# Kernel tuning notes

Hardware: AMD Instinct MI355X
Metric: run time of the kernel (lower is better)

## Reference

```python
import jax, jax.numpy as jnp
import numpy as np

T, B, N, DEG, F_IN, H, C = 48, 32, 96, 8, 16, 128, 500
E = B * N * DEG          # edges per timestep (already batch-offset within [0, B*N))
M = T * B * N            # total nodes across all timesteps
EPS = 1e-5               # BatchNorm eps


def setup_inputs() -> dict:
    key = jax.random.key(0)
    ks = jax.random.split(key, 24)
    rn = lambda k, s: jax.random.normal(k, s, dtype=jnp.float32) * 0.05
    return {
        "x": jax.random.normal(ks[0], (T, B * N, F_IN), dtype=jnp.float32),
        "edge_index": jax.random.randint(ks[1], (T, 2, E), 0, B * N, dtype=jnp.int32),
        "gcn_w0": rn(ks[2], (F_IN, H)),
        "gcn_w12": rn(ks[3], (2, H, H)),
        "gcn_b": rn(ks[4], (3, H)),
        "bn_gamma": jnp.ones((3, H), dtype=jnp.float32),
        "bn_beta": jnp.zeros((3, H), dtype=jnp.float32),
        "bn_mean": rn(ks[5], (3, H)),
        "bn_var": jax.random.uniform(ks[6], (3, H), minval=0.5, maxval=1.5, dtype=jnp.float32),
        "lstm_wih0": rn(ks[7], (2, 4 * H, H)),
        "lstm_whh0": rn(ks[8], (2, 4 * H, H)),
        "lstm_bih0": rn(ks[9], (2, 4 * H)),
        "lstm_bhh0": rn(ks[10], (2, 4 * H)),
        "lstm_wih1": rn(ks[11], (2, 4 * H, 2 * H)),
        "lstm_whh1": rn(ks[12], (2, 4 * H, H)),
        "lstm_bih1": rn(ks[13], (2, 4 * H)),
        "lstm_bhh1": rn(ks[14], (2, 4 * H)),
        "attn_w1": rn(ks[15], (2 * H, H)),
        "attn_b1": rn(ks[16], (H,)),
        "attn_w2": rn(ks[17], (H, 1)),
        "attn_b2": rn(ks[18], (1,)),
        "fc1_w": rn(ks[19], (2 * H, H)),
        "fc1_b": rn(ks[20], (H,)),
        "fc2_w": rn(ks[21], (H, C)),
        "fc2_b": rn(ks[22], (C,)),
    }


def _lstm_dir(x, wih, whh, bih, bhh):
    # x: [T, B, I]; PyTorch gate order i, f, g, o
    pre = jnp.einsum('tbi,gi->tbg', x, wih) + bih  # input projection hoisted out of scan
    h0 = jnp.zeros((x.shape[1], whh.shape[1]), x.dtype)

    def step(carry, p):
        h, c = carry
        g = p + h @ whh.T + bhh
        i, f, gg, o = jnp.split(g, 4, axis=-1)
        c = jax.nn.sigmoid(f) * c + jax.nn.sigmoid(i) * jnp.tanh(gg)
        h = jax.nn.sigmoid(o) * jnp.tanh(c)
        return (h, c), h

    _, hs = jax.lax.scan(step, (h0, h0), pre)
    return hs  # [T, B, Hh]


def _bilstm(x, wih, whh, bih, bhh):
    fwd = _lstm_dir(x, wih[0], whh[0], bih[0], bhh[0])
    bwd = _lstm_dir(x[::-1], wih[1], whh[1], bih[1], bhh[1])[::-1]
    return jnp.concatenate([fwd, bwd], axis=-1)  # [T, B, 2H]


def reference(x, edge_index, gcn_w0, gcn_w12, gcn_b,
              bn_gamma, bn_beta, bn_mean, bn_var,
              lstm_wih0, lstm_whh0, lstm_bih0, lstm_bhh0,
              lstm_wih1, lstm_whh1, lstm_bih1, lstm_bhh1,
              attn_w1, attn_b1, attn_w2, attn_b2,
              fc1_w, fc1_b, fc2_w, fc2_b):
    # Fold timesteps into one big node set by offsetting indices by t*B*N
    off = (jnp.arange(T, dtype=jnp.int32) * (B * N))[:, None]
    src = (edge_index[:, 0] + off).reshape(-1)
    dst = (edge_index[:, 1] + off).reshape(-1)

    # GCN symmetric norm with self-loops: deg counts incoming edges + self-loop
    deg = jax.ops.segment_sum(jnp.ones_like(src, dtype=x.dtype), dst, num_segments=M) + 1.0
    dinv = jax.lax.rsqrt(deg)
    enorm = (dinv[src] * dinv[dst])[:, None]   # per-edge norm
    self_norm = (1.0 / deg)[:, None]           # self-loop norm

    h = x.reshape(M, F_IN)
    for l in range(3):
        W = gcn_w0 if l == 0 else gcn_w12[l - 1]
        hw = h @ W  # GCNConv applies linear first
        z = jax.ops.segment_sum(hw[src] * enorm, dst, num_segments=M) + hw * self_norm + gcn_b[l]
        # BatchNorm1d eval-mode (running stats), then ReLU, residual if shapes match
        z = (z - bn_mean[l]) * (bn_gamma[l] * jax.lax.rsqrt(bn_var[l] + EPS)) + bn_beta[l]
        z = jax.nn.relu(z)
        h = z + h if l > 0 else z  # dropout is identity in eval

    # global_mean_pool per graph (fixed N nodes per graph)
    emb = h.reshape(T, B, N, H).mean(axis=2)  # [T, B, H]

    out1 = _bilstm(emb, lstm_wih0, lstm_whh0, lstm_bih0, lstm_bhh0)
    out2 = _bilstm(out1, lstm_wih1, lstm_whh1, lstm_bih1, lstm_bhh1)
    lstm_out = out2.transpose(1, 0, 2)  # [B, T, 2H]

    a = jnp.tanh(lstm_out @ attn_w1 + attn_b1) @ attn_w2 + attn_b2  # [B, T, 1]
    w = jax.nn.softmax(a, axis=1)
    ws = jnp.sum(lstm_out * w, axis=1)  # [B, 2H]

    y = jax.nn.relu(ws @ fc1_w + fc1_b) @ fc2_w + fc2_b
    return jax.nn.log_softmax(y, axis=1)
```

## Files before the change

### kernel.cpp

```cpp
#include <hip/hip_runtime.h>

#define T_ 48
#define B_ 32
#define N_ 96
#define E_ 24576
#define BN_ (B_*N_)
#define M_ (T_*BN_)
#define FIN_ 16
#define H_ 128
#define C_ 500
#define TE_ (T_*E_)
#define EPS_ 1e-5f

typedef _Float16 f16x8 __attribute__((ext_vector_type(8)));
typedef float    f32x4 __attribute__((ext_vector_type(4)));
typedef _Float16 half2v __attribute__((ext_vector_type(2)));

__device__ __forceinline__ ushort f2h(float f) {
    _Float16 h = (_Float16)f;
    union { _Float16 h; ushort u; } v;
    v.h = h;
    return v.u;
}
__device__ __forceinline__ float h2f(ushort u) {
    union { ushort u; _Float16 h; } v;
    v.u = u;
    return (float)v.h;
}
__device__ __forceinline__ half2v pkfma(unsigned int v, unsigned int w, half2v acc) {
#if __has_builtin(__builtin_elementwise_fma)
    return __builtin_elementwise_fma(__builtin_bit_cast(half2v, v),
                                     __builtin_bit_cast(half2v, w), acc);
#else
    half2v hv = __builtin_bit_cast(half2v, v);
    half2v wv = __builtin_bit_cast(half2v, w);
    acc[0] += hv[0]*wv[0];
    acc[1] += hv[1]*wv[1];
    return acc;
#endif
}
__device__ __forceinline__ float dot2pk(unsigned int hbits, unsigned int wbits, float acc) {
#if __has_builtin(__builtin_amdgcn_fdot2)
    return __builtin_amdgcn_fdot2(__builtin_bit_cast(half2v, hbits),
                                  __builtin_bit_cast(half2v, wbits), acc, false);
#else
    half2v hv = __builtin_bit_cast(half2v, hbits);
    half2v wv = __builtin_bit_cast(half2v, wbits);
    acc = fmaf((float)hv[0], (float)wv[0], acc);
    acc = fmaf((float)hv[1], (float)wv[1], acc);
    return acc;
#endif
}
__device__ __forceinline__ float sigm(float x) {
    return 1.f / (1.f + __expf(-x));
}
__device__ __forceinline__ float ftanh(float x) {
    x = fminf(15.f, fmaxf(-15.f, x));
    float e = __expf(2.f * x);
    return (e - 1.f) / (e + 1.f);
}

__global__ __launch_bounds__(1024) void csr_build_k(
    const int* __restrict__ ei, int* __restrict__ csr_off,
    unsigned int* __restrict__ csr_pk, float* __restrict__ dinv)
{
    int t = blockIdx.x;
    int tid = threadIdx.x;
    __shared__ int cnt[BN_];
    __shared__ int cur[BN_];
    __shared__ int scanbuf[1024];
    __shared__ unsigned int pk[E_];

    #pragma unroll
    for (int i = 0; i < 3; i++) cnt[tid + i*1024] = 0;
    __syncthreads();

    const int* srcp = ei + ((long)t*2+0)*E_;
    const int* dstp = ei + ((long)t*2+1)*E_;
    #pragma unroll
    for (int i = 0; i < E_/1024; i++)
        atomicAdd(&cnt[dstp[tid + i*1024]], 1);
    __syncthreads();

    int n0 = tid*3;
    int a = cnt[n0], b = cnt[n0+1], c = cnt[n0+2];
    int tot = a + b + c;
    scanbuf[tid] = tot;
    __syncthreads();
    for (int d = 1; d < 1024; d <<= 1) {
        int add = (tid >= d) ? scanbuf[tid-d] : 0;
        __syncthreads();
        scanbuf[tid] += add;
        __syncthreads();
    }
    int excl = scanbuf[tid] - tot;
    cur[n0] = excl; cur[n0+1] = excl + a; cur[n0+2] = excl + a + b;
    int gbase = t*BN_, ebase = t*E_;
    csr_off[gbase+n0]   = ebase + excl;
    csr_off[gbase+n0+1] = ebase + excl + a;
    csr_off[gbase+n0+2] = ebase + excl + a + b;
    dinv[gbase+n0]   = rsqrtf((float)a + 1.f);
    dinv[gbase+n0+1] = rsqrtf((float)b + 1.f);
    dinv[gbase+n0+2] = rsqrtf((float)c + 1.f);
    if (t == T_-1 && tid == 0) csr_off[M_] = TE_;
    __syncthreads();

    #pragma unroll
    for (int i = 0; i < E_/1024; i++) {
        int e = tid + i*1024;
        int s = srcp[e], d = dstp[e];
        int pos = atomicAdd(&cur[d], 1);
        float w = rsqrtf((float)cnt[s] + 1.f) * rsqrtf((float)cnt[d] + 1.f);
        pk[pos] = (unsigned int)s | ((unsigned int)f2h(w) << 16);
    }
    __syncthreads();

    uint4* dpk = (uint4*)(csr_pk + ebase);
    const uint4* spk = (const uint4*)pk;
    #pragma unroll
    for (int i = 0; i < E_/4096; i++)
        dpk[tid + i*1024] = spk[tid + i*1024];
}

#define WPREP_TOTAL (384+1024+4096+16384+16384+65536+65536+131072+262144)
__global__ void wprep_k(
    const float* __restrict__ gcn_b, const float* __restrict__ gam,
    const float* __restrict__ bet, const float* __restrict__ mu,
    const float* __restrict__ var,
    float* __restrict__ bn_sc, float* __restrict__ bn_sh,
    const float* __restrict__ bih0, const float* __restrict__ bhh0,
    float* __restrict__ bias0,
    const float* __restrict__ bih1, const float* __restrict__ bhh1,
    float* __restrict__ bias1,
    const float* __restrict__ gcn_w0, const float* __restrict__ gcn_w12,
    ushort* __restrict__ w0t, ushort* __restrict__ w1t, ushort* __restrict__ w2t,
    const float* __restrict__ whh0, const float* __restrict__ whh1,
    unsigned int* __restrict__ wpk0, unsigned int* __restrict__ wpk1,
    const float* __restrict__ wih0, const float* __restrict__ wih1,
    ushort* __restrict__ wih0b, ushort* __restrict__ wih1b)
{
    int i = blockIdx.x * blockDim.x + threadIdx.x;
    if (i >= WPREP_TOTAL) return;
    if (i < 384) {
        float sc = gam[i] * rsqrtf(var[i] + EPS_);
        bn_sc[i] = sc;
        bn_sh[i] = gcn_b[i]*sc + bet[i] - mu[i]*sc;
        return;
    }
    i -= 384;
    if (i < 1024) {
        bias0[i] = bih0[i] + bhh0[i];
        bias1[i] = bih1[i] + bhh1[i];
        return;
    }
    i -= 1024;
    if (i < 4096) {
        int e = i & 7, lane = (i >> 3) & 63, ct = i >> 9;
        int k = (lane >> 4)*8 + e;
        int c = ct*16 + (lane & 15);
        w0t[i] = (k < 16) ? f2h(gcn_w0[k*128 + c]) : (ushort)0;
        return;
    }
    i -= 4096;
    if (i < 16384) {
        int e = i & 7, lane = (i >> 3) & 63, kk = (i >> 9) & 3, ct = i >> 11;
        int k = kk*32 + (lane >> 4)*8 + e;
        int c = ct*16 + (lane & 15);
        w1t[i] = f2h(gcn_w12[k*128 + c]);
        return;
    }
    i -= 16384;
    if (i < 16384) {
        int e = i & 7, lane = (i >> 3) & 63, kk = (i >> 9) & 3, ct = i >> 11;
        int k = kk*32 + (lane >> 4)*8 + e;
        int c = ct*16 + (lane & 15);
        w2t[i] = f2h(gcn_w12[16384 + k*128 + c]);
        return;
    }
    i -= 16384;
    if (i < 65536) {
        int dir = i >> 15, r = i & 32767;
        int ab = r >> 14, r2 = r & 16383;
        int q = r2 >> 8, tidw = r2 & 255;
        int hh = tidw >> 1, gp = tidw & 1;
        int g = (2*gp + ab)*128 + hh;
        const float* wr = whh0 + ((long)(dir*512 + g))*128 + 2*q;
        wpk0[i] = (unsigned int)f2h(wr[0]) | ((unsigned int)f2h(wr[1]) << 16);
        return;
    }
    i -= 65536;
    if (i < 65536) {
        int dir = i >> 15, r = i & 32767;
        int ab = r >> 14, r2 = r & 16383;
        int q = r2 >> 8, tidw = r2 & 255;
        int hh = tidw >> 1, gp = tidw & 1;
        int g = (2*gp + ab)*128 + hh;
        const float* wr = whh1 + ((long)(dir*512 + g))*128 + 2*q;
        wpk1[i] = (unsigned int)f2h(wr[0]) | ((unsigned int)f2h(wr[1]) << 16);
        return;
    }
    i -= 65536;
    if (i < 131072) {
        int dir = i >> 16, r = i & 0xFFFF;
        int nt = r >> 11, kk = (r >> 9) & 3, lane = (r >> 3) & 63, e = r & 7;
        int n = nt*16 + (lane & 15);
        int k = kk*32 + (lane >> 4)*8 + e;
        wih0b[i] = f2h(wih0[((long)dir*512 + n)*128 + k]);
        return;
    }
    i -= 131072;
    {
        int dir = i >> 17, r = i & 0x1FFFF;
        int nt = r >> 12, kk = (r >> 9) & 7, lane = (r >> 3) & 63, e = r & 7;
        int n = nt*16 + (lane & 15);
        int k = kk*32 + (lane >> 4)*8 + e;
        wih1b[i] = f2h(wih1[((long)dir*512 + n)*256 + k]);
    }
}

__global__ __launch_bounds__(256) void gcn_layer_k(
    const ushort* __restrict__ h, const ushort* __restrict__ Wt,
    ushort* __restrict__ Cout,
    const int* __restrict__ csr_off, const unsigned int* __restrict__ csr_pk,
    const float* __restrict__ dinv,
    const float* __restrict__ bnsc, const float* __restrict__ bnsh)
{
    __shared__ ushort agg[64][136];
    int nb = gridDim.x;
    int chunk = nb >> 3;
    int bswz = (blockIdx.x & 7) * chunk + (blockIdx.x >> 3);
    int base = bswz * 64;
    int tbase = (base / BN_) * BN_;
    int wv = threadIdx.x >> 6;
    int lane = threadIdx.x & 63;
    int l2 = lane * 2;

    for (int pass = 0; pass < 8; pass++) {
        int nodeA = __builtin_amdgcn_readfirstlane(base + pass*8 + wv*2);
        int e00 = __builtin_amdgcn_readfirstlane(csr_off[nodeA]);
        int e01 = __builtin_amdgcn_readfirstlane(csr_off[nodeA+1]);
        int e11 = __builtin_amdgcn_readfirstlane(csr_off[nodeA+2]);
        int dA = e01 - e00, dB = e11 - e01;
        unsigned int mypkA = (lane < dA) ? csr_pk[e00 + lane] : 0u;
        unsigned int mypkB = (lane < dB) ? csr_pk[e01 + lane] : 0u;
        float dvA = dinv[nodeA], dvB = dinv[nodeA+1];
        unsigned int selfA = *(const unsigned int*)(h + (size_t)nodeA*128 + l2);
        unsigned int selfB = *(const unsigned int*)(h + (size_t)(nodeA+1)*128 + l2);

        ushort swA = f2h(dvA * dvA), swB = f2h(dvB * dvB);
        half2v spA = __builtin_bit_cast(half2v, (unsigned int)(swA * 0x10001u));
        half2v spB = __builtin_bit_cast(half2v, (unsigned int)(swB * 0x10001u));
        half2v a0 = __builtin_bit_cast(half2v, selfA);
        a0[0] *= spA[0]; a0[1] *= spA[1];
        half2v b0 = __builtin_bit_cast(half2v, selfB);
        b0[0] *= spB[0]; b0[1] *= spB[1];
        half2v a1 = {(_Float16)0.f, (_Float16)0.f}, a2 = a1, a3 = a1;
        half2v b1 = a1, b2 = a1, b3 = a1;

        int cA = (dA < 64) ? dA : 64;
        int cB = (dB < 64) ? dB : 64;
        int cA4 = cA & ~3, cB4 = cB & ~3;
        int cm = (cA4 > cB4) ? cA4 : cB4;
        for (int j = 0; j < cm; j += 4) {
            unsigned int pA0, pA1, pA2, pA3, vA0, vA1, vA2, vA3;
            unsigned int pB0, pB1, pB2, pB3, vB0, vB1, vB2, vB3;
            bool qA = (j < cA4), qB = (j < cB4);
            if (qA) {
                pA0 = (unsigned int)__builtin_amdgcn_readlane((int)mypkA, j+0);
                pA1 = (unsigned int)__builtin_amdgcn_readlane((int)mypkA, j+1);
                pA2 = (unsigned int)__builtin_amdgcn_readlane((int)mypkA, j+2);
                pA3 = (unsigned int)__builtin_amdgcn_readlane((int)mypkA, j+3);
                vA0 = *(const unsigned int*)(h + (size_t)(tbase + (int)(pA0 & 0xffffu))*128 + l2);
                vA1 = *(const unsigned int*)(h + (size_t)(tbase + (int)(pA1 & 0xffffu))*128 + l2);
                vA2 = *(const unsigned int*)(h + (size_t)(tbase + (int)(pA2 & 0xffffu))*128 + l2);
                vA3 = *(const unsigned int*)(h + (size_t)(tbase + (int)(pA3 & 0xffffu))*128 + l2);
            }
            if (qB) {
                pB0 = (unsigned int)__builtin_amdgcn_readlane((int)mypkB, j+0);
                pB1 = (unsigned int)__builtin_amdgcn_readlane((int)mypkB, j+1);
                pB2 = (unsigned int)__builtin_amdgcn_readlane((int)mypkB, j+2);
                pB3 = (unsigned int)__builtin_amdgcn_readlane((int)mypkB, j+3);
                vB0 = *(const unsigned int*)(h + (size_t)(tbase + (int)(pB0 & 0xffffu))*128 + l2);
                vB1 = *(const unsigned int*)(h + (size_t)(tbase + (int)(pB1 & 0xffffu))*128 + l2);
                vB2 = *(const unsigned int*)(h + (size_t)(tbase + (int)(pB2 & 0xffffu))*128 + l2);
                vB3 = *(const unsigned int*)(h + (size_t)(tbase + (int)(pB3 & 0xffffu))*128 + l2);
            }
            if (qA) {
                a0 = pkfma(vA0, (pA0 >> 16) * 0x10001u, a0);
                a1 = pkfma(vA1, (pA1 >> 16) * 0x10001u, a1);
                a2 = pkfma(vA2, (pA2 >> 16) * 0x10001u, a2);
                a3 = pkfma(vA3, (pA3 >> 16) * 0x10001u, a3);
            }
            if (qB) {
                b0 = pkfma(vB0, (pB0 >> 16) * 0x10001u, b0);
                b1 = pkfma(vB1, (pB1 >> 16) * 0x10001u, b1);
                b2 = pkfma(vB2, (pB2 >> 16) * 0x10001u, b2);
                b3 = pkfma(vB3, (pB3 >> 16) * 0x10001u, b3);
            }
        }
        for (int j = cA4; j < cA; j++) {
            unsigned int pk0 = (unsigned int)__builtin_amdgcn_readlane((int)mypkA, j);
            unsigned int v = *(const unsigned int*)(h + (size_t)(tbase + (int)(pk0 & 0xffffu))*128 + l2);
            a0 = pkfma(v, (pk0 >> 16) * 0x10001u, a0);
        }
        for (int j = cB4; j < cB; j++) {
            unsigned int pk0 = (unsigned int)__builtin_amdgcn_readlane((int)mypkB, j);
            unsigned int v = *(const unsigned int*)(h + (size_t)(tbase + (int)(pk0 & 0xffffu))*128 + l2);
            b0 = pkfma(v, (pk0 >> 16) * 0x10001u, b0);
        }
        for (int jj = e00 + 64; jj < e01; jj++) {
            unsigned int pk0 = __builtin_amdgcn_readfirstlane(csr_pk[jj]);
            unsigned int v = *(const unsigned int*)(h + (size_t)(tbase + (int)(pk0 & 0xffffu))*128 + l2);
            a0 = pkfma(v, (pk0 >> 16) * 0x10001u, a0);
        }
        for (int jj = e01 + 64; jj < e11; jj++) {
            unsigned int pk0 = __builtin_amdgcn_readfirstlane(csr_pk[jj]);
            unsigned int v = *(const unsigned int*)(h + (size_t)(tbase + (int)(pk0 & 0xffffu))*128 + l2);
            b0 = pkfma(v, (pk0 >> 16) * 0x10001u, b0);
        }
        float ra0 = ((float)a0[0] + (float)a1[0]) + ((float)a2[0] + (float)a3[0]);
        float ra1 = ((float)a0[1] + (float)a1[1]) + ((float)a2[1] + (float)a3[1]);
        float rb0 = ((float)b0[0] + (float)b1[0]) + ((float)b2[0] + (float)b3[0]);
        float rb1 = ((float)b0[1] + (float)b1[1]) + ((float)b2[1] + (float)b3[1]);
        int nlA = nodeA - base;
        *(unsigned int*)&agg[nlA][l2] =
            (unsigned int)f2h(ra0) | ((unsigned int)f2h(ra1) << 16);
        *(unsigned int*)&agg[nlA+1][l2] =
            (unsigned int)f2h(rb0) | ((unsigned int)f2h(rb1) << 16);
    }
    __syncthreads();

    int l16 = lane & 15, lh = lane >> 4;
    f32x4 acc[8];
    #pragma unroll
    for (int i = 0; i < 8; i++) acc[i] = (f32x4){0.f, 0.f, 0.f, 0.f};
    #pragma unroll
    for (int kk = 0; kk < 4; kk++) {
        f16x8 af = *reinterpret_cast<const f16x8*>(&agg[wv*16 + l16][kk*32 + lh*8]);
        #pragma unroll
        for (int ct = 0; ct < 8; ct++) {
            f16x8 bfr = *reinterpret_cast<const f16x8*>(
                &Wt[(((long)ct*4 + kk)*64 + lane)*8]);
            acc[ct] = __builtin_amdgcn_mfma_f32_16x16x32_f16(af, bfr, acc[ct], 0, 0, 0);
        }
    }
    __syncthreads();

    #pragma unroll
    for (int ct = 0; ct < 8; ct++) {
        int col = ct*16 + l16;
        float sc = bnsc[col], sh = bnsh[col];
        #pragma unroll
        for (int r = 0; r < 4; r++) {
            int rl = wv*16 + lh*4 + r;
            float v = acc[ct][r] * sc + sh;
            agg[rl][col] = f2h(fmaxf(v, 0.f));
        }
    }
    __syncthreads();
    long rowblock = (long)base;
    #pragma unroll
    for (int it = 0; it < 4; it++) {
        int s = it*256 + threadIdx.x;
        int rl = s >> 4, c8 = (s & 15) * 8;
        uint4 v = *(const uint4*)&agg[rl][c8];
        uint4 rv = *(const uint4*)&h[(rowblock + rl)*128 + c8];
        half2v* vv = (half2v*)&v;
        const half2v* rr = (const half2v*)&rv;
        vv[0] += rr[0]; vv[1] += rr[1]; vv[2] += rr[2]; vv[3] += rr[3];
        *(uint4*)&Cout[(rowblock + rl)*128 + c8] = v;
    }
}

__global__ __launch_bounds__(256) void gcn0_k(
    const float* __restrict__ x, const ushort* __restrict__ Wt,
    ushort* __restrict__ Cout,
    const int* __restrict__ csr_off, const unsigned int* __restrict__ csr_pk,
    const float* __restrict__ dinv,
    const float* __restrict__ bnsc, const float* __restrict__ bnsh)
{
    __shared__ ushort agg[64][32];
    __shared__ ushort cl[64][136];
    int tid = threadIdx.x;
    int nl = tid >> 2;
    int fq = tid & 3;
    int f0 = fq*4;
    int node = blockIdx.x*64 + nl;
    int tbase = (node / BN_) * BN_;
    float dv = dinv[node];
    float4 sv = *(const float4*)(x + (long)node*16 + f0);
    float s = dv*dv;
    float a0 = sv.x*s, a1 = sv.y*s, a2 = sv.z*s, a3 = sv.w*s;
    int e0 = csr_off[node], e1 = csr_off[node+1];
    int j = e0;
    for (; j + 4 <= e1; j += 4) {
        unsigned int p0 = csr_pk[j], p1 = csr_pk[j+1], p2 = csr_pk[j+2], p3 = csr_pk[j+3];
        int s0 = tbase + (int)(p0 & 0xffffu), s1 = tbase + (int)(p1 & 0xffffu);
        int s2 = tbase + (int)(p2 & 0xffffu), s3 = tbase + (int)(p3 & 0xffffu);
        float w0 = h2f((ushort)(p0 >> 16)), w1 = h2f((ushort)(p1 >> 16));
        float w2 = h2f((ushort)(p2 >> 16)), w3 = h2f((ushort)(p3 >> 16));
        float4 v0 = *(const float4*)(x + (long)s0*16 + f0);
        float4 v1 = *(const float4*)(x + (long)s1*16 + f0);
        float4 v2 = *(const float4*)(x + (long)s2*16 + f0);
        float4 v3 = *(const float4*)(x + (long)s3*16 + f0);
        a0 += v0.x*w0 + v1.x*w1 + v2.x*w2 + v3.x*w3;
        a1 += v0.y*w0 + v1.y*w1 + v2.y*w2 + v3.y*w3;
        a2 += v0.z*w0 + v1.z*w1 + v2.z*w2 + v3.z*w3;
        a3 += v0.w*w0 + v1.w*w1 + v2.w*w2 + v3.w*w3;
    }
    for (; j < e1; j++) {
        unsigned int pk0 = csr_pk[j];
        int sc = tbase + (int)(pk0 & 0xffffu);
        float en = h2f((ushort)(pk0 >> 16));
        float4 v = *(const float4*)(x + (long)sc*16 + f0);
        a0 += v.x*en; a1 += v.y*en; a2 += v.z*en; a3 += v.w*en;
    }
    agg[nl][f0+0] = f2h(a0);
    agg[nl][f0+1] = f2h(a1);
    agg[nl][f0+2] = f2h(a2);
    agg[nl][f0+3] = f2h(a3);
    agg[nl][16+f0+0] = 0;
    agg[nl][16+f0+1] = 0;
    agg[nl][16+f0+2] = 0;
    agg[nl][16+f0+3] = 0;
    __syncthreads();

    int w = tid >> 6, lane = tid & 63;
    int l16 = lane & 15, lh = lane >> 4;
    f16x8 af = *reinterpret_cast<const f16x8*>(&agg[w*16 + l16][lh*8]);
    f32x4 acc[8];
    #pragma unroll
    for (int i = 0; i < 8; i++) acc[i] = (f32x4){0.f, 0.f, 0.f, 0.f};
    #pragma unroll
    for (int ct = 0; ct < 8; ct++) {
        f16x8 bfr = *reinterpret_cast<const f16x8*>(&Wt[((long)ct*64 + lane)*8]);
        acc[ct] = __builtin_amdgcn_mfma_f32_16x16x32_f16(af, bfr, acc[ct], 0, 0, 0);
    }

    #pragma unroll
    for (int ct = 0; ct < 8; ct++) {
        int col = ct*16 + l16;
        float sc = bnsc[col], sh = bnsh[col];
        #pragma unroll
        for (int r = 0; r < 4; r++) {
            int rl = w*16 + lh*4 + r;
            float v = acc[ct][r] * sc + sh;
            cl[rl][col] = f2h(fmaxf(v, 0.f));
        }
    }
    __syncthreads();
    long rowblock = (long)blockIdx.x * 64;
    #pragma unroll
    for (int it = 0; it < 4; it++) {
        int ss = it*256 + tid;
        int rl = ss >> 4, c8 = (ss & 15) * 8;
        uint4 v = *(const uint4*)&cl[rl][c8];
        *(uint4*)&Cout[(rowblock + rl)*128 + c8] = v;
    }
}

template<int K>
__global__ __launch_bounds__(256) void mm_pre_k(
    const ushort* __restrict__ A, const ushort* __restrict__ Wt_all,
    float* __restrict__ Cout_all, const float* __restrict__ bias_all)
{
    constexpr int KST = K/32;
    int dir = blockIdx.z;
    const ushort* Wt = Wt_all + (size_t)dir * 512 * K;
    float* Cout = Cout_all + (size_t)dir * T_ * B_ * 512;
    const float* bias = bias_all + dir * 512;

    int tid = threadIdx.x;
    int w = tid >> 6, lane = tid & 63;
    int l16 = lane & 15, lh = lane >> 4;
    int row0 = blockIdx.x * 64 + w * 16;
    int nt0 = blockIdx.y * 8;

    f32x4 acc[8];
    #pragma unroll
    for (int i = 0; i < 8; i++) acc[i] = (f32x4){0.f, 0.f, 0.f, 0.f};

    #pragma unroll
    for (int kk = 0; kk < KST; kk++) {
        int ka = kk*32 + lh*8;
        f16x8 af = *reinterpret_cast<const f16x8*>(&A[(long)(row0 + l16)*K + ka]);
        #pragma unroll
        for (int ct = 0; ct < 8; ct++) {
            f16x8 bfr = *reinterpret_cast<const f16x8*>(
                &Wt[(((long)(nt0 + ct)*KST + kk)*64 + lane)*8]);
            acc[ct] = __builtin_amdgcn_mfma_f32_16x16x32_f16(af, bfr, acc[ct], 0, 0, 0);
        }
    }

    #pragma unroll
    for (int ct = 0; ct < 8; ct++) {
        int col = (nt0 + ct)*16 + l16;
        float bv = bias[col];
        int gate = col >> 7, hh = col & 127;
        int colp = (gate & 1)*256 + hh*2 + (gate >> 1);
        #pragma unroll
        for (int r = 0; r < 4; r++) {
            int row = row0 + lh*4 + r;
            Cout[(long)row*512 + colp] = acc[ct][r] + bv;
        }
    }
}


__global__ void meanpool_k(const ushort* __restrict__ h, ushort* __restrict__ embb) {
    int row = blockIdx.x;
    int t = row / B_, b = row - t*B_;
    int hh = threadIdx.x;
    const ushort* base = h + ((long)t*BN_ + b*N_)*H_ + hh;
    float acc = 0.f;
    for (int n = 0; n < N_; n++) acc += h2f(base[(long)n*H_]);
    embb[(long)row*H_ + hh] = f2h(acc * (1.f / N_));
}

__global__ __launch_bounds__(256) void lstm_scan_k(
    const float* __restrict__ pre,
    const unsigned int* __restrict__ wpkbuf,
    float* __restrict__ out,
    ushort* __restrict__ outb)
{
    int dir = blockIdx.x >> 5;
    int b   = blockIdx.x & 31;
    int tid = threadIdx.x;
    int gp  = tid & 1;
    int hh  = tid >> 1;

    __shared__ ushort hbuf[2][H_];
    ((ushort*)hbuf)[tid] = 0;
    float creg = 0.f;

    const unsigned int* wpA = wpkbuf + ((long)dir*2 + 0)*64*256;
    const unsigned int* wpB = wpkbuf + ((long)dir*2 + 1)*64*256;
    unsigned int wA[64], wB[64];
    #pragma unroll
    for (int q = 0; q < 64; q++) {
        wA[q] = wpA[q*256 + tid];
        wB[q] = wpB[q*256 + tid];
    }

    const float* pred = pre + (long)dir * T_ * B_ * 512;
    int t = dir ? (T_ - 1) : 0;
    int tstep = dir ? -1 : 1;
    float pvA = pred[(((long)t*B_ + b)*2 + 0)*256 + tid];
    float pvB = pred[(((long)t*B_ + b)*2 + 1)*256 + tid];
    __syncthreads();

    for (int st = 0; st < T_; st++) {
        int tn = t + tstep;
        tn = (tn < 0) ? 0 : ((tn >= T_) ? T_ - 1 : tn);
        float pvAn = pred[(((long)tn*B_ + b)*2 + 0)*256 + tid];
        float pvBn = pred[(((long)tn*B_ + b)*2 + 1)*256 + tid];

        const uint4* h4 = (const uint4*)hbuf[st & 1];
        float a0 = pvA, a1 = 0.f, a2 = 0.f, a3 = 0.f;
        float c0 = pvB, c1 = 0.f, c2 = 0.f, c3 = 0.f;
        #pragma unroll
        for (int jj = 0; jj < 16; jj++) {
            uint4 hv = h4[jj];
            a0 = dot2pk(hv.x, wA[jj*4+0], a0);
            a1 = dot2pk(hv.y, wA[jj*4+1], a1);
            a2 = dot2pk(hv.z, wA[jj*4+2], a2);
            a3 = dot2pk(hv.w, wA[jj*4+3], a3);
            c0 = dot2pk(hv.x, wB[jj*4+0], c0);
            c1 = dot2pk(hv.y, wB[jj*4+1], c1);
            c2 = dot2pk(hv.z, wB[jj*4+2], c2);
            c3 = dot2pk(hv.w, wB[jj*4+3], c3);
        }
        float sA = (a0 + a1) + (a2 + a3);
        float sB = (c0 + c1) + (c2 + c3);
        float oA = __shfl_xor(sA, 1, 64);
        float oB = __shfl_xor(sB, 1, 64);
        float ig = gp ? oA : sA;
        float fg = gp ? oB : sB;
        float gg = gp ? sA : oA;
        float og = gp ? sB : oB;
        float c = sigm(fg) * creg + sigm(ig) * ftanh(gg);
        float h = sigm(og) * ftanh(c);
        creg = c;
        if (gp == 0) {
            hbuf[(st + 1) & 1][hh] = f2h(h);
            long orow = ((long)t*B_ + b)*256 + dir*H_ + hh;
            if (out)  out[orow] = h;
            if (outb) outb[orow] = f2h(h);
        }
        __syncthreads();
        pvA = pvAn; pvB = pvBn;
        t = tn;
    }
}


__global__ __launch_bounds__(128) void attn_a_k(
    const ushort* __restrict__ out2, const float* __restrict__ w1,
    const float* __restrict__ b1, const float* __restrict__ w2,
    const float* __restrict__ b2v, float* __restrict__ a)
{
    int row = blockIdx.x;
    int j = threadIdx.x;
    const ushort* xr = out2 + (long)row * 256;
    float acc = b1[j];
    for (int k = 0; k < 256; k++) acc += h2f(xr[k]) * w1[k*128 + j];
    float u = tanhf(acc) * w2[j];
    __shared__ float red[128];
    red[j] = u;
    __syncthreads();
    for (int d = 64; d > 0; d >>= 1) {
        if (j < d) red[j] += red[j + d];
        __syncthreads();
    }
    if (j == 0) {
        int t = row / B_, b = row - t*B_;
        a[b*T_ + t] = red[0] + b2v[0];
    }
}

__global__ __launch_bounds__(256) void attn_pool_k(
    const ushort* __restrict__ out2, const float* __restrict__ a,
    float* __restrict__ wsv)
{
    int b = blockIdx.x;
    __shared__ float w[T_];
    if (threadIdx.x == 0) {
        float m = -1e30f;
        for (int t = 0; t < T_; t++) m = fmaxf(m, a[b*T_ + t]);
        float s = 0.f;
        for (int t = 0; t < T_; t++) { float e = __expf(a[b*T_ + t] - m); w[t] = e; s += e; }
        float inv = 1.f / s;
        for (int t = 0; t < T_; t++) w[t] *= inv;
    }
    __syncthreads();
    int h2 = threadIdx.x;
    float acc = 0.f;
    for (int t = 0; t < T_; t++) acc += w[t] * h2f(out2[((long)t*B_ + b)*256 + h2]);
    wsv[b*256 + h2] = acc;
}


__global__ __launch_bounds__(512) void head_k(
    const float* __restrict__ wsv, const float* __restrict__ w1,
    const float* __restrict__ b1, const float* __restrict__ w2,
    const float* __restrict__ b2, float* __restrict__ outp)
{
    int b = blockIdx.x;
    int tid = threadIdx.x;
    __shared__ float r[128];
    __shared__ float y[C_];
    __shared__ float red[512];
    if (tid < 128) {
        float acc = b1[tid];
        for (int k = 0; k < 256; k++) acc += wsv[b*256 + k] * w1[k*128 + tid];
        r[tid] = fmaxf(acc, 0.f);
    }
    __syncthreads();
    for (int c = tid; c < C_; c += 512) {
        float acc = b2[c];
        for (int k = 0; k < 128; k++) acc += r[k] * w2[k*C_ + c];
        y[c] = acc;
    }
    __syncthreads();
    float m = -1e30f;
    for (int c = tid; c < C_; c += 512) m = fmaxf(m, y[c]);
    red[tid] = m;
    __syncthreads();
    for (int d = 256; d > 0; d >>= 1) {
        if (tid < d) red[tid] = fmaxf(red[tid], red[tid + d]);
        __syncthreads();
    }
    m = red[0];
    __syncthreads();
    float s = 0.f;
    for (int c = tid; c < C_; c += 512) s += __expf(y[c] - m);
    red[tid] = s;
    __syncthreads();
    for (int d = 256; d > 0; d >>= 1) {
        if (tid < d) red[tid] += red[tid + d];
        __syncthreads();
    }
    float lse = m + logf(red[0]);
    for (int c = tid; c < C_; c += 512) outp[(long)b*C_ + c] = y[c] - lse;
}


extern "C" void kernel_launch(void* const* d_in, const int* in_sizes, int n_in,
                              void* d_out, int out_size, void* d_ws, size_t ws_size,
                              hipStream_t stream) {
    const float* x        = (const float*)d_in[0];
    const int*   ei       = (const int*)d_in[1];
    const float* gcn_w0   = (const float*)d_in[2];
    const float* gcn_w12  = (const float*)d_in[3];
    const float* gcn_b    = (const float*)d_in[4];
    const float* bn_gamma = (const float*)d_in[5];
    const float* bn_beta  = (const float*)d_in[6];
    const float* bn_mean  = (const float*)d_in[7];
    const float* bn_var   = (const float*)d_in[8];
    const float* wih0     = (const float*)d_in[9];
    const float* whh0     = (const float*)d_in[10];
    const float* bih0     = (const float*)d_in[11];
    const float* bhh0     = (const float*)d_in[12];
    const float* wih1     = (const float*)d_in[13];
    const float* whh1     = (const float*)d_in[14];
    const float* bih1     = (const float*)d_in[15];
    const float* bhh1     = (const float*)d_in[16];
    const float* attn_w1  = (const float*)d_in[17];
    const float* attn_b1  = (const float*)d_in[18];
    const float* attn_w2  = (const float*)d_in[19];
    const float* attn_b2  = (const float*)d_in[20];
    const float* fc1_w    = (const float*)d_in[21];
    const float* fc1_b    = (const float*)d_in[22];
    const float* fc2_w    = (const float*)d_in[23];
    const float* fc2_b    = (const float*)d_in[24];

    char* p = (char*)d_ws;
    auto alloc = [&](size_t bytes) {
        void* r = (void*)p;
        p += (bytes + 255) & ~(size_t)255;
        return r;
    };
    ushort* hbA    = (ushort*)alloc((size_t)M_*H_*2);
    ushort* hbB    = (ushort*)alloc((size_t)M_*H_*2);
    float* dinv    = (float*)alloc((size_t)M_*4);
    int*   csr_off = (int*)  alloc((size_t)(M_+1)*4);
    unsigned int* csr_pk = (unsigned int*)alloc((size_t)TE_*4);
    float* bn_sc   = (float*)alloc(384*4);
    float* bn_sh   = (float*)alloc(384*4);
    float* bias0   = (float*)alloc(1024*4);
    float* bias1   = (float*)alloc(1024*4);
    ushort* w0t    = (ushort*)alloc((size_t)4096*2);
    ushort* w1t    = (ushort*)alloc((size_t)16384*2);
    ushort* w2t    = (ushort*)alloc((size_t)16384*2);
    unsigned int* wpk0 = (unsigned int*)alloc((size_t)2*64*512*4);
    unsigned int* wpk1 = (unsigned int*)alloc((size_t)2*64*512*4);
    ushort* wih0b  = (ushort*)alloc((size_t)2*512*128*2);
    ushort* wih1b  = (ushort*)alloc((size_t)2*512*256*2);
    ushort* embb   = (ushort*)alloc((size_t)T_*B_*H_*2);
    float* pre     = (float*)alloc((size_t)2*T_*B_*512*4);
    ushort* out1b  = (ushort*)alloc((size_t)T_*B_*256*2);
    ushort* out2b  = (ushort*)alloc((size_t)T_*B_*256*2);
    float* attn_av = (float*)alloc((size_t)B_*T_*4);
    float* wsv     = (float*)alloc((size_t)B_*256*4);

    csr_build_k<<<T_, 1024, 0, stream>>>(ei, csr_off, csr_pk, dinv);

    wprep_k<<<(WPREP_TOTAL+255)/256, 256, 0, stream>>>(
        gcn_b, bn_gamma, bn_beta, bn_mean, bn_var, bn_sc, bn_sh,
        bih0, bhh0, bias0, bih1, bhh1, bias1,
        gcn_w0, gcn_w12, w0t, w1t, w2t,
        whh0, whh1, wpk0, wpk1,
        wih0, wih1, wih0b, wih1b);

    gcn0_k<<<M_/64, 256, 0, stream>>>(x, w0t, hbA, csr_off, csr_pk, dinv,
                                      bn_sc + 0, bn_sh + 0);
    gcn_layer_k<<<M_/64, 256, 0, stream>>>(hbA, w1t, hbB, csr_off, csr_pk, dinv,
                                           bn_sc + 128, bn_sh + 128);
    gcn_layer_k<<<M_/64, 256, 0, stream>>>(hbB, w2t, hbA, csr_off, csr_pk, dinv,
                                           bn_sc + 256, bn_sh + 256);

    meanpool_k<<<T_*B_, 128, 0, stream>>>(hbA, embb);

    mm_pre_k<128><<<dim3((T_*B_)/64, 4, 2), 256, 0, stream>>>(embb, wih0b, pre, bias0);
    lstm_scan_k<<<64, 256, 0, stream>>>(pre, wpk0, nullptr, out1b);

    mm_pre_k<256><<<dim3((T_*B_)/64, 4, 2), 256, 0, stream>>>(out1b, wih1b, pre, bias1);
    lstm_scan_k<<<64, 256, 0, stream>>>(pre, wpk1, nullptr, out2b);

    attn_a_k<<<T_*B_, 128, 0, stream>>>(out2b, attn_w1, attn_b1, attn_w2, attn_b2, attn_av);
    attn_pool_k<<<B_, 256, 0, stream>>>(out2b, attn_av, wsv);

    head_k<<<B_, 512, 0, stream>>>(wsv, fc1_w, fc1_b, fc2_w, fc2_b, (float*)d_out);
}
```

Baseline: 301.4 us.

## Double GCN layer block to 512 threads and derive self-loop norm from degree

The GCN layer kernel now runs 8 waves per block instead of 4. Each wave aggregates fewer nodes per pass, and the MFMA output columns are split across wave pairs, so each wave keeps 4 accumulators instead of 8. The precomputed dinv array is removed, and the self-loop weight is computed as 1/(deg+1) from the CSR offsets, which saves a global array write and read. The larger block raises parallelism within each block and lowers register pressure, but may reduce how many blocks fit per CU.

```diff
diff --git a/kernel.cpp b/kernel.cpp
--- a/kernel.cpp
+++ b/kernel.cpp
@@ -62,7 +62,7 @@
 
 __global__ __launch_bounds__(1024) void csr_build_k(
     const int* __restrict__ ei, int* __restrict__ csr_off,
-    unsigned int* __restrict__ csr_pk, float* __restrict__ dinv)
+    unsigned int* __restrict__ csr_pk)
 {
     int t = blockIdx.x;
     int tid = threadIdx.x;
@@ -99,9 +99,6 @@
     csr_off[gbase+n0]   = ebase + excl;
     csr_off[gbase+n0+1] = ebase + excl + a;
     csr_off[gbase+n0+2] = ebase + excl + a + b;
-    dinv[gbase+n0]   = rsqrtf((float)a + 1.f);
-    dinv[gbase+n0+1] = rsqrtf((float)b + 1.f);
-    dinv[gbase+n0+2] = rsqrtf((float)c + 1.f);
     if (t == T_-1 && tid == 0) csr_off[M_] = TE_;
     __syncthreads();
 
@@ -218,11 +215,10 @@
     }
 }
 
-__global__ __launch_bounds__(256) void gcn_layer_k(
+__global__ __launch_bounds__(512) void gcn_layer_k(
     const ushort* __restrict__ h, const ushort* __restrict__ Wt,
     ushort* __restrict__ Cout,
     const int* __restrict__ csr_off, const unsigned int* __restrict__ csr_pk,
-    const float* __restrict__ dinv,
     const float* __restrict__ bnsc, const float* __restrict__ bnsh)
 {
     __shared__ ushort agg[64][136];
@@ -235,19 +231,21 @@
     int lane = threadIdx.x & 63;
     int l2 = lane * 2;
 
-    for (int pass = 0; pass < 8; pass++) {
-        int nodeA = __builtin_amdgcn_readfirstlane(base + pass*8 + wv*2);
+    #pragma unroll
+    for (int pass = 0; pass < 4; pass++) {
+        int nlA = pass*16 + wv*2;
+        int nodeA = __builtin_amdgcn_readfirstlane(base + nlA);
         int e00 = __builtin_amdgcn_readfirstlane(csr_off[nodeA]);
         int e01 = __builtin_amdgcn_readfirstlane(csr_off[nodeA+1]);
         int e11 = __builtin_amdgcn_readfirstlane(csr_off[nodeA+2]);
         int dA = e01 - e00, dB = e11 - e01;
         unsigned int mypkA = (lane < dA) ? csr_pk[e00 + lane] : 0u;
         unsigned int mypkB = (lane < dB) ? csr_pk[e01 + lane] : 0u;
-        float dvA = dinv[nodeA], dvB = dinv[nodeA+1];
         unsigned int selfA = *(const unsigned int*)(h + (size_t)nodeA*128 + l2);
         unsigned int selfB = *(const unsigned int*)(h + (size_t)(nodeA+1)*128 + l2);
 
-        ushort swA = f2h(dvA * dvA), swB = f2h(dvB * dvB);
+        ushort swA = f2h(1.0f / (float)(dA + 1));
+        ushort swB = f2h(1.0f / (float)(dB + 1));
         half2v spA = __builtin_bit_cast(half2v, (unsigned int)(swA * 0x10001u));
         half2v spB = __builtin_bit_cast(half2v, (unsigned int)(swB * 0x10001u));
         half2v a0 = __builtin_bit_cast(half2v, selfA);
@@ -322,7 +320,6 @@
         float ra1 = ((float)a0[1] + (float)a1[1]) + ((float)a2[1] + (float)a3[1]);
         float rb0 = ((float)b0[0] + (float)b1[0]) + ((float)b2[0] + (float)b3[0]);
         float rb1 = ((float)b0[1] + (float)b1[1]) + ((float)b2[1] + (float)b3[1]);
-        int nlA = nodeA - base;
         *(unsigned int*)&agg[nlA][l2] =
             (unsigned int)f2h(ra0) | ((unsigned int)f2h(ra1) << 16);
         *(unsigned int*)&agg[nlA+1][l2] =
@@ -331,37 +328,40 @@
     __syncthreads();
 
     int l16 = lane & 15, lh = lane >> 4;
-    f32x4 acc[8];
-    #pragma unroll
-    for (int i = 0; i < 8; i++) acc[i] = (f32x4){0.f, 0.f, 0.f, 0.f};
+    int rowgrp = wv >> 1;
+    int chalf = (wv & 1) * 4;
+    f32x4 acc[4];
+    #pragma unroll
+    for (int i = 0; i < 4; i++) acc[i] = (f32x4){0.f, 0.f, 0.f, 0.f};
     #pragma unroll
     for (int kk = 0; kk < 4; kk++) {
-        f16x8 af = *reinterpret_cast<const f16x8*>(&agg[wv*16 + l16][kk*32 + lh*8]);
+        f16x8 af = *reinterpret_cast<const f16x8*>(&agg[rowgrp*16 + l16][kk*32 + lh*8]);
         #pragma unroll
-        for (int ct = 0; ct < 8; ct++) {
+        for (int c4 = 0; c4 < 4; c4++) {
+            int ct = chalf + c4;
             f16x8 bfr = *reinterpret_cast<const f16x8*>(
                 &Wt[(((long)ct*4 + kk)*64 + lane)*8]);
-            acc[ct] = __builtin_amdgcn_mfma_f32_16x16x32_f16(af, bfr, acc[ct], 0, 0, 0);
-        }
-    }
-    __syncthreads();
-
-    #pragma unroll
-    for (int ct = 0; ct < 8; ct++) {
-        int col = ct*16 + l16;
+            acc[c4] = __builtin_amdgcn_mfma_f32_16x16x32_f16(af, bfr, acc[c4], 0, 0, 0);
+        }
+    }
+    __syncthreads();
+
+    #pragma unroll
+    for (int c4 = 0; c4 < 4; c4++) {
+        int col = (chalf + c4)*16 + l16;
         float sc = bnsc[col], sh = bnsh[col];
         #pragma unroll
         for (int r = 0; r < 4; r++) {
-            int rl = wv*16 + lh*4 + r;
-            float v = acc[ct][r] * sc + sh;
+            int rl = rowgrp*16 + lh*4 + r;
+            float v = acc[c4][r] * sc + sh;
             agg[rl][col] = f2h(fmaxf(v, 0.f));
         }
     }
     __syncthreads();
     long rowblock = (long)base;
     #pragma unroll
-    for (int it = 0; it < 4; it++) {
-        int s = it*256 + threadIdx.x;
+    for (int it = 0; it < 2; it++) {
+        int s = it*512 + threadIdx.x;
         int rl = s >> 4, c8 = (s & 15) * 8;
         uint4 v = *(const uint4*)&agg[rl][c8];
         uint4 rv = *(const uint4*)&h[(rowblock + rl)*128 + c8];
@@ -376,7 +376,6 @@
     const float* __restrict__ x, const ushort* __restrict__ Wt,
     ushort* __restrict__ Cout,
     const int* __restrict__ csr_off, const unsigned int* __restrict__ csr_pk,
-    const float* __restrict__ dinv,
     const float* __restrict__ bnsc, const float* __restrict__ bnsh)
 {
     __shared__ ushort agg[64][32];
@@ -387,11 +386,10 @@
     int f0 = fq*4;
     int node = blockIdx.x*64 + nl;
     int tbase = (node / BN_) * BN_;
-    float dv = dinv[node];
+    int e0 = csr_off[node], e1 = csr_off[node+1];
+    float s = 1.0f / (float)(e1 - e0 + 1);
     float4 sv = *(const float4*)(x + (long)node*16 + f0);
-    float s = dv*dv;
     float a0 = sv.x*s, a1 = sv.y*s, a2 = sv.z*s, a3 = sv.w*s;
-    int e0 = csr_off[node], e1 = csr_off[node+1];
     int j = e0;
     for (; j + 4 <= e1; j += 4) {
         unsigned int p0 = csr_pk[j], p1 = csr_pk[j+1], p2 = csr_pk[j+2], p3 = csr_pk[j+3];
@@ -722,7 +720,6 @@
     };
     ushort* hbA    = (ushort*)alloc((size_t)M_*H_*2);
     ushort* hbB    = (ushort*)alloc((size_t)M_*H_*2);
-    float* dinv    = (float*)alloc((size_t)M_*4);
     int*   csr_off = (int*)  alloc((size_t)(M_+1)*4);
     unsigned int* csr_pk = (unsigned int*)alloc((size_t)TE_*4);
     float* bn_sc   = (float*)alloc(384*4);
@@ -743,7 +740,7 @@
     float* attn_av = (float*)alloc((size_t)B_*T_*4);
     float* wsv     = (float*)alloc((size_t)B_*256*4);
 
-    csr_build_k<<<T_, 1024, 0, stream>>>(ei, csr_off, csr_pk, dinv);
+    csr_build_k<<<T_, 1024, 0, stream>>>(ei, csr_off, csr_pk);
 
     wprep_k<<<(WPREP_TOTAL+255)/256, 256, 0, stream>>>(
         gcn_b, bn_gamma, bn_beta, bn_mean, bn_var, bn_sc, bn_sh,
@@ -752,11 +749,11 @@
         whh0, whh1, wpk0, wpk1,
         wih0, wih1, wih0b, wih1b);
 
-    gcn0_k<<<M_/64, 256, 0, stream>>>(x, w0t, hbA, csr_off, csr_pk, dinv,
+    gcn0_k<<<M_/64, 256, 0, stream>>>(x, w0t, hbA, csr_off, csr_pk,
                                       bn_sc + 0, bn_sh + 0);
-    gcn_layer_k<<<M_/64, 256, 0, stream>>>(hbA, w1t, hbB, csr_off, csr_pk, dinv,
+    gcn_layer_k<<<M_/64, 512, 0, stream>>>(hbA, w1t, hbB, csr_off, csr_pk,
                                            bn_sc + 128, bn_sh + 128);
-    gcn_layer_k<<<M_/64, 256, 0, stream>>>(hbB, w2t, hbA, csr_off, csr_pk, dinv,
+    gcn_layer_k<<<M_/64, 512, 0, stream>>>(hbB, w2t, hbA, csr_off, csr_pk,
                                            bn_sc + 256, bn_sh + 256);
 
     meanpool_k<<<T_*B_, 128, 0, stream>>>(hbA, embb);
```

After: 275.9 us. 1.09x faster.
